# Performance work log

Hardware: AMD Instinct MI355X
Metric: run time of the kernel (lower is better)

Reference implementation:

```python
import jax, jax.numpy as jnp
import numpy as np

B, N, M, D = 256, 256, 256, 1024
BIG = 1e30  # stands in for +inf; far larger than any reachable DTW cost (<= 2*N)


def setup_inputs() -> dict:
    key = jax.random.key(0)
    k1, k2 = jax.random.split(key)
    seq1 = jax.random.normal(k1, (B, N, D), dtype=jnp.float32)
    seq2 = jax.random.normal(k2, (B, M, D), dtype=jnp.float32)
    return {"seq1": seq1, "seq2": seq2}


def _cosine_distance(x, y):
    # F.normalize(p=2, dim=2) with eps=1e-12, then 1 - clamp(x_n @ y_n^T, -1, 1)
    xn = x / jnp.maximum(jnp.linalg.norm(x, axis=2, keepdims=True), 1e-12)
    yn = y / jnp.maximum(jnp.linalg.norm(y, axis=2, keepdims=True), 1e-12)
    sim = jnp.einsum('bnd,bmd->bnm', xn, yn)
    return 1.0 - jnp.clip(sim, -1.0, 1.0)


def _dtw(dist, band_radius):
    # Banded (Sakoe-Chiba) DTW DP: acc[i,j] = d[i,j] + min(acc[i-1,j], acc[i,j-1], acc[i-1,j-1])
    # Row-wise lax.scan; within-row recurrence a[j] = min(b[j], a[j-1] + s[j]) is a
    # min-plus linear recurrence, solved in parallel with lax.associative_scan.
    b, n, m = dist.shape
    jdx = jnp.arange(m)
    # row 0: cumulative sum inside band (j <= r), BIG outside
    row0 = jnp.where(jdx[None, :] <= band_radius, jnp.cumsum(dist[:, 0, :], axis=1), BIG)

    def step(prev, xs):
        i, di = xs  # di: [b, m] = dist[:, i, :]
        in_band = (jdx >= 1) & (jdx >= i - band_radius) & (jdx <= i + band_radius)
        # column 0 only initialized while i <= band_radius (matches torch loop)
        a0 = jnp.where(i <= band_radius, prev[:, 0] + di[:, 0], BIG)
        prev_shift = jnp.concatenate([jnp.full((b, 1), BIG, dist.dtype), prev[:, :-1]], axis=1)
        c = jnp.minimum(prev, prev_shift)  # min(acc[i-1,j], acc[i-1,j-1])
        bt = jnp.where(in_band[None, :], c + di, BIG)
        st = jnp.where(in_band[None, :], di, BIG)

        def comb(l, r):
            sl, tl = l
            sr, tr = r
            return (sl + sr, jnp.minimum(tr, tl + sr))

        ss, tt = jax.lax.associative_scan(comb, (st[:, 1:], bt[:, 1:]), axis=1)
        row = jnp.concatenate([a0[:, None], jnp.minimum(tt, a0[:, None] + ss)], axis=1)
        return row, None

    xs = (jnp.arange(1, n), jnp.swapaxes(dist[:, 1:, :], 0, 1))  # ([n-1], [n-1,b,m])
    last_row, _ = jax.lax.scan(step, row0, xs)
    return last_row[:, m - 1]


def reference(seq1, seq2):
    dist = _cosine_distance(seq1, seq2)
    band_radius = min(N, M) // 2  # default: half of shorter sequence
    return _dtw(dist, band_radius)
```

## Files before the change

### kernel.cpp

```cpp
#include <hip/hip_runtime.h>
#include <hip/hip_bf16.h>

#define B_ 256
#define N_ 256
#define M_ 256
#define D_ 1024
#define RAD 128
#define BIGF 1e30f

typedef short bf16x8 __attribute__((ext_vector_type(8)));
typedef float f32x4 __attribute__((ext_vector_type(4)));

__device__ __forceinline__ short f2bf(float f) {
    __hip_bfloat16 h = __float2bfloat16(f);
    return __builtin_bit_cast(short, h);
}

__device__ __forceinline__ void cvt4(const float4 v, short* s, float& n) {
    n += v.x * v.x + v.y * v.y + v.z * v.z + v.w * v.w;
    s[0] = f2bf(v.x); s[1] = f2bf(v.y); s[2] = f2bf(v.z); s[3] = f2bf(v.w);
}

__global__ __launch_bounds__(256) void gemm_dist_kernel(
        const float* __restrict__ X, const float* __restrict__ Y,
        float* __restrict__ dist) {
    const int bid = blockIdx.x;
    const int b  = bid >> 2;
    const int ti = (bid >> 1) & 1;
    const int tj = bid & 1;

    __shared__ short As[128][32];
    __shared__ short Bs[128][32];
    __shared__ float redA[256];
    __shared__ float redB[256];
    __shared__ float rnx[128];
    __shared__ float rny[128];

    const int t    = threadIdx.x;
    const int row  = t >> 1;
    const int kh   = (t & 1) << 4;
    const int wave = t >> 6;
    const int lane = t & 63;
    const int wi   = (wave >> 1) << 6;
    const int wj   = (wave & 1) << 6;
    const int fq   = lane >> 4;
    const int fr   = lane & 15;

    const float* ax = X + (((size_t)b * N_ + ti * 128 + row) * D_) + kh;
    const float* by = Y + (((size_t)b * M_ + tj * 128 + row) * D_) + kh;

    f32x4 acc[4][4];
    const f32x4 zero = {0.f, 0.f, 0.f, 0.f};
#pragma unroll
    for (int r = 0; r < 4; ++r)
#pragma unroll
        for (int c = 0; c < 4; ++c) acc[r][c] = zero;

    float nA = 0.f, nB = 0.f;

    for (int kt = 0; kt < D_ / 32; ++kt) {
        const float4 va0 = *(const float4*)(ax + 0);
        const float4 va1 = *(const float4*)(ax + 4);
        const float4 va2 = *(const float4*)(ax + 8);
        const float4 va3 = *(const float4*)(ax + 12);
        const float4 vb0 = *(const float4*)(by + 0);
        const float4 vb1 = *(const float4*)(by + 4);
        const float4 vb2 = *(const float4*)(by + 8);
        const float4 vb3 = *(const float4*)(by + 12);
        ax += 32; by += 32;

        short sa[16], sb[16];
        cvt4(va0, sa + 0,  nA); cvt4(va1, sa + 4,  nA);
        cvt4(va2, sa + 8,  nA); cvt4(va3, sa + 12, nA);
        cvt4(vb0, sb + 0,  nB); cvt4(vb1, sb + 4,  nB);
        cvt4(vb2, sb + 8,  nB); cvt4(vb3, sb + 12, nB);

        __syncthreads();
        *(bf16x8*)&As[row][kh]     = *(bf16x8*)&sa[0];
        *(bf16x8*)&As[row][kh + 8] = *(bf16x8*)&sa[8];
        *(bf16x8*)&Bs[row][kh]     = *(bf16x8*)&sb[0];
        *(bf16x8*)&Bs[row][kh + 8] = *(bf16x8*)&sb[8];
        __syncthreads();

        bf16x8 af[4], bf[4];
#pragma unroll
        for (int r = 0; r < 4; ++r)
            af[r] = *(const bf16x8*)&As[wi + r * 16 + fr][fq * 8];
#pragma unroll
        for (int c = 0; c < 4; ++c)
            bf[c] = *(const bf16x8*)&Bs[wj + c * 16 + fr][fq * 8];
#pragma unroll
        for (int r = 0; r < 4; ++r)
#pragma unroll
            for (int c = 0; c < 4; ++c)
                acc[r][c] = __builtin_amdgcn_mfma_f32_16x16x32_bf16(
                    af[r], bf[c], acc[r][c], 0, 0, 0);
    }

    redA[t] = nA;
    redB[t] = nB;
    __syncthreads();
    if (t < 128) {
        float sA = redA[2 * t] + redA[2 * t + 1];
        float sB = redB[2 * t] + redB[2 * t + 1];
        rnx[t] = 1.0f / fmaxf(sqrtf(sA), 1e-12f);
        rny[t] = 1.0f / fmaxf(sqrtf(sB), 1e-12f);
    }
    __syncthreads();

    float* Dp = dist + (((size_t)b * N_ + ti * 128) * M_) + tj * 128;
#pragma unroll
    for (int r = 0; r < 4; ++r) {
#pragma unroll
        for (int c = 0; c < 4; ++c) {
            const int col = wj + c * 16 + fr;
            const float rc = rny[col];
#pragma unroll
            for (int g = 0; g < 4; ++g) {
                const int rw = wi + r * 16 + fq * 4 + g;
                float v = acc[r][c][g] * rnx[rw] * rc;
                v = fminf(1.0f, fmaxf(-1.0f, v));
                Dp[(size_t)rw * M_ + col] = 1.0f - v;
            }
        }
    }
}

__global__ __launch_bounds__(64) void dtw_kernel(
        const float* __restrict__ dist, float* __restrict__ out) {
    const int b = blockIdx.x;
    const int lane = threadIdx.x;
    const float* Db = dist + (size_t)b * N_ * M_;
    const int j0 = lane << 2;

    float4 d = *(const float4*)(Db + j0);
    float s0 = d.x, s1 = s0 + d.y, s2 = s1 + d.z, s3 = s2 + d.w;
    float tot = s3;
#pragma unroll
    for (int off = 1; off < 64; off <<= 1) {
        float o = __shfl_up(tot, off);
        if (lane >= off) tot += o;
    }
    float excl = __shfl_up(tot, 1);
    if (lane == 0) excl = 0.f;
    float prev[4];
    prev[0] = (j0 + 0 <= RAD) ? excl + s0 : BIGF;
    prev[1] = (j0 + 1 <= RAD) ? excl + s1 : BIGF;
    prev[2] = (j0 + 2 <= RAD) ? excl + s2 : BIGF;
    prev[3] = (j0 + 3 <= RAD) ? excl + s3 : BIGF;

    float4 dn = *(const float4*)(Db + M_ + j0);

    for (int i = 1; i < N_; ++i) {
        d = dn;
        if (i + 1 < N_) dn = *(const float4*)(Db + (size_t)(i + 1) * M_ + j0);

        const float pm1 = __shfl_up(prev[3], 1);
        const float p00 = __shfl(prev[0], 0);
        const float d00 = __shfl(d.x, 0);
        const float a0 = (i <= RAD) ? p00 + d00 : BIGF;

        const float de[4] = {d.x, d.y, d.z, d.w};
        const float ps[4] = {pm1, prev[0], prev[1], prev[2]};

        float S = 0.f, T = BIGF;
        float Se[4], Te[4];
#pragma unroll
        for (int e = 0; e < 4; ++e) {
            const int j = j0 + e;
            float st, bt;
            if (j == 0) {
                st = 0.f; bt = BIGF;
            } else {
                const bool in = (j >= i - RAD) && (j <= i + RAD);
                const float c = fminf(prev[e], ps[e]);
                bt = in ? c + de[e] : BIGF;
                st = in ? de[e] : BIGF;
            }
            T = fminf(bt, T + st);
            S = S + st;
            Se[e] = S; Te[e] = T;
        }

        float iS = S, iT = T;
#pragma unroll
        for (int off = 1; off < 64; off <<= 1) {
            float oS = __shfl_up(iS, off);
            float oT = __shfl_up(iT, off);
            if (lane >= off) {
                iT = fminf(iT, oT + iS);
                iS = oS + iS;
            }
        }
        float eS = __shfl_up(iS, 1);
        float eT = __shfl_up(iT, 1);
        if (lane == 0) { eS = 0.f; eT = BIGF; }

#pragma unroll
        for (int e = 0; e < 4; ++e) {
            const float fS = eS + Se[e];
            const float fT = fminf(Te[e], eT + Se[e]);
            prev[e] = fminf(fT, a0 + fS);
        }
        if (lane == 0) prev[0] = a0;
    }

    if (lane == 63) out[b] = prev[3];
}

extern "C" void kernel_launch(void* const* d_in, const int* in_sizes, int n_in,
                              void* d_out, int out_size, void* d_ws, size_t ws_size,
                              hipStream_t stream) {
    const float* seq1 = (const float*)d_in[0];
    const float* seq2 = (const float*)d_in[1];
    float* out = (float*)d_out;
    float* dist = (float*)d_ws;

    hipLaunchKernelGGL(gemm_dist_kernel, dim3(B_ * 4), dim3(256), 0, stream,
                       seq1, seq2, dist);
    hipLaunchKernelGGL(dtw_kernel, dim3(B_), dim3(64), 0, stream, dist, out);
}
```

Baseline: 682.4 us.

## Double-buffer padded LDS tiles and prefetch global loads in distance GEMM

The GEMM main loop now keeps two LDS buffers, unrolled two k-tiles per iteration, and needs only one barrier per tile instead of two. It also loads the next tile's global data into registers before staging the current one, so memory latency overlaps the MFMA work. LDS rows are padded from 32 to 40 shorts to cut bank conflicts on fragment reads. The norm-reduction scratch now reuses the A tile buffer to offset the larger LDS footprint. The cost is more registers held by the prefetched tiles, which may reduce occupancy.

```diff
diff --git a/kernel.cpp b/kernel.cpp
--- a/kernel.cpp
+++ b/kernel.cpp
@@ -7,6 +7,7 @@
 #define D_ 1024
 #define RAD 128
 #define BIGF 1e30f
+#define LDK 40
 
 typedef short bf16x8 __attribute__((ext_vector_type(8)));
 typedef float f32x4 __attribute__((ext_vector_type(4)));
@@ -19,6 +20,21 @@
 __device__ __forceinline__ void cvt4(const float4 v, short* s, float& n) {
     n += v.x * v.x + v.y * v.y + v.z * v.z + v.w * v.w;
     s[0] = f2bf(v.x); s[1] = f2bf(v.y); s[2] = f2bf(v.z); s[3] = f2bf(v.w);
+}
+
+struct Pk { float4 a0, a1, a2, a3, b0, b1, b2, b3; };
+
+__device__ __forceinline__ Pk loadpk(const float* ax, const float* by) {
+    Pk p;
+    p.a0 = *(const float4*)(ax + 0);
+    p.a1 = *(const float4*)(ax + 4);
+    p.a2 = *(const float4*)(ax + 8);
+    p.a3 = *(const float4*)(ax + 12);
+    p.b0 = *(const float4*)(by + 0);
+    p.b1 = *(const float4*)(by + 4);
+    p.b2 = *(const float4*)(by + 8);
+    p.b3 = *(const float4*)(by + 12);
+    return p;
 }
 
 __global__ __launch_bounds__(256) void gemm_dist_kernel(
@@ -29,12 +45,8 @@
     const int ti = (bid >> 1) & 1;
     const int tj = bid & 1;
 
-    __shared__ short As[128][32];
-    __shared__ short Bs[128][32];
-    __shared__ float redA[256];
-    __shared__ float redB[256];
-    __shared__ float rnx[128];
-    __shared__ float rny[128];
+    __shared__ alignas(16) short As[2][128][LDK];
+    __shared__ alignas(16) short Bs[2][128][LDK];
 
     const int t    = threadIdx.x;
     const int row  = t >> 1;
@@ -58,55 +70,58 @@
 
     float nA = 0.f, nB = 0.f;
 
-    for (int kt = 0; kt < D_ / 32; ++kt) {
-        const float4 va0 = *(const float4*)(ax + 0);
-        const float4 va1 = *(const float4*)(ax + 4);
-        const float4 va2 = *(const float4*)(ax + 8);
-        const float4 va3 = *(const float4*)(ax + 12);
-        const float4 vb0 = *(const float4*)(by + 0);
-        const float4 vb1 = *(const float4*)(by + 4);
-        const float4 vb2 = *(const float4*)(by + 8);
-        const float4 vb3 = *(const float4*)(by + 12);
-        ax += 32; by += 32;
-
+    auto stage = [&](const Pk& p, int buf) {
         short sa[16], sb[16];
-        cvt4(va0, sa + 0,  nA); cvt4(va1, sa + 4,  nA);
-        cvt4(va2, sa + 8,  nA); cvt4(va3, sa + 12, nA);
-        cvt4(vb0, sb + 0,  nB); cvt4(vb1, sb + 4,  nB);
-        cvt4(vb2, sb + 8,  nB); cvt4(vb3, sb + 12, nB);
-
+        cvt4(p.a0, sa + 0,  nA); cvt4(p.a1, sa + 4,  nA);
+        cvt4(p.a2, sa + 8,  nA); cvt4(p.a3, sa + 12, nA);
+        cvt4(p.b0, sb + 0,  nB); cvt4(p.b1, sb + 4,  nB);
+        cvt4(p.b2, sb + 8,  nB); cvt4(p.b3, sb + 12, nB);
+
+        *(bf16x8*)&As[buf][row][kh]     = *(bf16x8*)&sa[0];
+        *(bf16x8*)&As[buf][row][kh + 8] = *(bf16x8*)&sa[8];
+        *(bf16x8*)&Bs[buf][row][kh]     = *(bf16x8*)&sb[0];
+        *(bf16x8*)&Bs[buf][row][kh + 8] = *(bf16x8*)&sb[8];
         __syncthreads();
-        *(bf16x8*)&As[row][kh]     = *(bf16x8*)&sa[0];
-        *(bf16x8*)&As[row][kh + 8] = *(bf16x8*)&sa[8];
-        *(bf16x8*)&Bs[row][kh]     = *(bf16x8*)&sb[0];
-        *(bf16x8*)&Bs[row][kh + 8] = *(bf16x8*)&sb[8];
-        __syncthreads();
-
-        bf16x8 af[4], bf[4];
+
+        bf16x8 af[4], bfr[4];
 #pragma unroll
         for (int r = 0; r < 4; ++r)
-            af[r] = *(const bf16x8*)&As[wi + r * 16 + fr][fq * 8];
+            af[r] = *(const bf16x8*)&As[buf][wi + r * 16 + fr][fq * 8];
 #pragma unroll
         for (int c = 0; c < 4; ++c)
-            bf[c] = *(const bf16x8*)&Bs[wj + c * 16 + fr][fq * 8];
+            bfr[c] = *(const bf16x8*)&Bs[buf][wj + c * 16 + fr][fq * 8];
 #pragma unroll
         for (int r = 0; r < 4; ++r)
 #pragma unroll
             for (int c = 0; c < 4; ++c)
                 acc[r][c] = __builtin_amdgcn_mfma_f32_16x16x32_bf16(
-                    af[r], bf[c], acc[r][c], 0, 0, 0);
-    }
-
-    redA[t] = nA;
-    redB[t] = nB;
+                    af[r], bfr[c], acc[r][c], 0, 0, 0);
+    };
+
+    Pk cur = loadpk(ax, by); ax += 32; by += 32;
+    for (int kt = 0; kt < D_ / 32; kt += 2) {
+        Pk nxt = loadpk(ax, by); ax += 32; by += 32;
+        stage(cur, 0);
+        if (kt + 2 < D_ / 32) {
+            cur = loadpk(ax, by); ax += 32; by += 32;
+        }
+        stage(nxt, 1);
+    }
+
+    __syncthreads();
+    float* scratch = (float*)&As[0][0][0];
+    scratch[t]       = nA;
+    scratch[256 + t] = nB;
     __syncthreads();
     if (t < 128) {
-        float sA = redA[2 * t] + redA[2 * t + 1];
-        float sB = redB[2 * t] + redB[2 * t + 1];
-        rnx[t] = 1.0f / fmaxf(sqrtf(sA), 1e-12f);
-        rny[t] = 1.0f / fmaxf(sqrtf(sB), 1e-12f);
+        float sA = scratch[2 * t] + scratch[2 * t + 1];
+        float sB = scratch[256 + 2 * t] + scratch[256 + 2 * t + 1];
+        scratch[512 + t] = 1.0f / fmaxf(sqrtf(sA), 1e-12f);
+        scratch[640 + t] = 1.0f / fmaxf(sqrtf(sB), 1e-12f);
     }
     __syncthreads();
+    const float* rnx = scratch + 512;
+    const float* rny = scratch + 640;
 
     float* Dp = dist + (((size_t)b * N_ + ti * 128) * M_) + tj * 128;
 #pragma unroll
```

Measured after the change: 663.8 us. 1.03x faster.

## Double-buffer GEMM tiles with direct global-to-LDS loads and swizzled layout

Applied to the files above, without the earlier changes.

The distance GEMM now stages fp32 tiles straight into double-buffered shared memory with global_load_lds, prefetching the next K-slice while computing the current one. Conversion to bf16 and the row-norm accumulation move to after the LDS read, and an XOR swizzle is meant to avoid bank conflicts. Block indices are remapped across XCDs and launch bounds request two blocks per CU. The cost is fp32 LDS tiles, which doubles shared-memory use and LDS read traffic, plus redundant bf16 conversions per wave.

```diff
diff --git a/kernel.cpp b/kernel.cpp
--- a/kernel.cpp
+++ b/kernel.cpp
@@ -16,38 +16,44 @@
     return __builtin_bit_cast(short, h);
 }
 
-__device__ __forceinline__ void cvt4(const float4 v, short* s, float& n) {
-    n += v.x * v.x + v.y * v.y + v.z * v.z + v.w * v.w;
-    s[0] = f2bf(v.x); s[1] = f2bf(v.y); s[2] = f2bf(v.z); s[3] = f2bf(v.w);
-}
-
-__global__ __launch_bounds__(256) void gemm_dist_kernel(
+#define GLL16(g, l)                                                        \
+    __builtin_amdgcn_global_load_lds(                                      \
+        (const __attribute__((address_space(1))) void*)(g),                \
+        (__attribute__((address_space(3))) void*)(l), 16, 0, 0)
+
+__global__ __launch_bounds__(256, 2) void gemm_dist_kernel(
         const float* __restrict__ X, const float* __restrict__ Y,
         float* __restrict__ dist) {
-    const int bid = blockIdx.x;
+    const int obid = blockIdx.x;
+    const int bid  = (obid & 7) * (B_ * 4 / 8) + (obid >> 3);
     const int b  = bid >> 2;
     const int ti = (bid >> 1) & 1;
     const int tj = bid & 1;
 
-    __shared__ short As[128][32];
-    __shared__ short Bs[128][32];
-    __shared__ float redA[256];
-    __shared__ float redB[256];
-    __shared__ float rnx[128];
-    __shared__ float rny[128];
+    __shared__ float Asf[2][128][32];
+    __shared__ float Bsf[2][128][32];
 
     const int t    = threadIdx.x;
-    const int row  = t >> 1;
-    const int kh   = (t & 1) << 4;
     const int wave = t >> 6;
     const int lane = t & 63;
     const int wi   = (wave >> 1) << 6;
     const int wj   = (wave & 1) << 6;
     const int fq   = lane >> 4;
     const int fr   = lane & 15;
-
-    const float* ax = X + (((size_t)b * N_ + ti * 128 + row) * D_) + kh;
-    const float* by = Y + (((size_t)b * M_ + tj * 128 + row) * D_) + kh;
+    const int sA   = fr & 7;
+
+    const int lr  = lane >> 3;
+    const int lg  = lane & 7;
+    const int gsw = (lg ^ lr) << 2;
+
+    const float* gA[4];
+    const float* gB[4];
+#pragma unroll
+    for (int i = 0; i < 4; ++i) {
+        const int c = wave * 4 + i;
+        gA[i] = X + ((size_t)(b * N_ + ti * 128 + c * 8 + lr)) * D_ + gsw;
+        gB[i] = Y + ((size_t)(b * M_ + tj * 128 + c * 8 + lr)) * D_ + gsw;
+    }
 
     f32x4 acc[4][4];
     const f32x4 zero = {0.f, 0.f, 0.f, 0.f};
@@ -56,55 +62,97 @@
 #pragma unroll
         for (int c = 0; c < 4; ++c) acc[r][c] = zero;
 
-    float nA = 0.f, nB = 0.f;
-
+    float nAr[4] = {0.f, 0.f, 0.f, 0.f};
+    float nBr[4] = {0.f, 0.f, 0.f, 0.f};
+
+    const int g0f = (((fq << 1) | 0) ^ sA) << 2;
+    const int g1f = (((fq << 1) | 1) ^ sA) << 2;
+
+    auto stage = [&](int buf, int kt) {
+#pragma unroll
+        for (int i = 0; i < 4; ++i) {
+            const int c = wave * 4 + i;
+            GLL16(gA[i] + kt * 32, &Asf[buf][c * 8][0]);
+            GLL16(gB[i] + kt * 32, &Bsf[buf][c * 8][0]);
+        }
+    };
+
+    stage(0, 0);
     for (int kt = 0; kt < D_ / 32; ++kt) {
-        const float4 va0 = *(const float4*)(ax + 0);
-        const float4 va1 = *(const float4*)(ax + 4);
-        const float4 va2 = *(const float4*)(ax + 8);
-        const float4 va3 = *(const float4*)(ax + 12);
-        const float4 vb0 = *(const float4*)(by + 0);
-        const float4 vb1 = *(const float4*)(by + 4);
-        const float4 vb2 = *(const float4*)(by + 8);
-        const float4 vb3 = *(const float4*)(by + 12);
-        ax += 32; by += 32;
-
-        short sa[16], sb[16];
-        cvt4(va0, sa + 0,  nA); cvt4(va1, sa + 4,  nA);
-        cvt4(va2, sa + 8,  nA); cvt4(va3, sa + 12, nA);
-        cvt4(vb0, sb + 0,  nB); cvt4(vb1, sb + 4,  nB);
-        cvt4(vb2, sb + 8,  nB); cvt4(vb3, sb + 12, nB);
-
-        __syncthreads();
-        *(bf16x8*)&As[row][kh]     = *(bf16x8*)&sa[0];
-        *(bf16x8*)&As[row][kh + 8] = *(bf16x8*)&sa[8];
-        *(bf16x8*)&Bs[row][kh]     = *(bf16x8*)&sb[0];
-        *(bf16x8*)&Bs[row][kh + 8] = *(bf16x8*)&sb[8];
-        __syncthreads();
-
-        bf16x8 af[4], bf[4];
-#pragma unroll
-        for (int r = 0; r < 4; ++r)
-            af[r] = *(const bf16x8*)&As[wi + r * 16 + fr][fq * 8];
-#pragma unroll
-        for (int c = 0; c < 4; ++c)
-            bf[c] = *(const bf16x8*)&Bs[wj + c * 16 + fr][fq * 8];
+        const int buf = kt & 1;
+        if (kt + 1 < D_ / 32) {
+            stage(buf ^ 1, kt + 1);
+            asm volatile("s_waitcnt vmcnt(8)" ::: "memory");
+        } else {
+            asm volatile("s_waitcnt vmcnt(0)" ::: "memory");
+        }
+        __builtin_amdgcn_s_barrier();
+        asm volatile("" ::: "memory");
+
+        const float (*Ab)[32] = Asf[buf];
+        const float (*Bb)[32] = Bsf[buf];
+
+        bf16x8 af[4], bfv[4];
+#pragma unroll
+        for (int r = 0; r < 4; ++r) {
+            const float* rp = &Ab[wi + r * 16 + fr][0];
+            const f32x4 lo = *(const f32x4*)(rp + g0f);
+            const f32x4 hi = *(const f32x4*)(rp + g1f);
+            if (wj == 0) {
+                nAr[r] += lo[0]*lo[0] + lo[1]*lo[1] + lo[2]*lo[2] + lo[3]*lo[3]
+                        + hi[0]*hi[0] + hi[1]*hi[1] + hi[2]*hi[2] + hi[3]*hi[3];
+            }
+            bf16x8 v;
+            v[0]=f2bf(lo[0]); v[1]=f2bf(lo[1]); v[2]=f2bf(lo[2]); v[3]=f2bf(lo[3]);
+            v[4]=f2bf(hi[0]); v[5]=f2bf(hi[1]); v[6]=f2bf(hi[2]); v[7]=f2bf(hi[3]);
+            af[r] = v;
+        }
+#pragma unroll
+        for (int c = 0; c < 4; ++c) {
+            const float* rp = &Bb[wj + c * 16 + fr][0];
+            const f32x4 lo = *(const f32x4*)(rp + g0f);
+            const f32x4 hi = *(const f32x4*)(rp + g1f);
+            if (wi == 0) {
+                nBr[c] += lo[0]*lo[0] + lo[1]*lo[1] + lo[2]*lo[2] + lo[3]*lo[3]
+                        + hi[0]*hi[0] + hi[1]*hi[1] + hi[2]*hi[2] + hi[3]*hi[3];
+            }
+            bf16x8 v;
+            v[0]=f2bf(lo[0]); v[1]=f2bf(lo[1]); v[2]=f2bf(lo[2]); v[3]=f2bf(lo[3]);
+            v[4]=f2bf(hi[0]); v[5]=f2bf(hi[1]); v[6]=f2bf(hi[2]); v[7]=f2bf(hi[3]);
+            bfv[c] = v;
+        }
+
 #pragma unroll
         for (int r = 0; r < 4; ++r)
 #pragma unroll
             for (int c = 0; c < 4; ++c)
                 acc[r][c] = __builtin_amdgcn_mfma_f32_16x16x32_bf16(
-                    af[r], bf[c], acc[r][c], 0, 0, 0);
-    }
-
-    redA[t] = nA;
-    redB[t] = nB;
+                    af[r], bfv[c], acc[r][c], 0, 0, 0);
+
+        asm volatile("" ::: "memory");
+        __builtin_amdgcn_s_barrier();
+    }
+
     __syncthreads();
-    if (t < 128) {
-        float sA = redA[2 * t] + redA[2 * t + 1];
-        float sB = redB[2 * t] + redB[2 * t + 1];
-        rnx[t] = 1.0f / fmaxf(sqrtf(sA), 1e-12f);
-        rny[t] = 1.0f / fmaxf(sqrtf(sB), 1e-12f);
+    float* rnx = (float*)&Asf[0][0][0];
+    float* rny = rnx + 128;
+    if (wj == 0) {
+#pragma unroll
+        for (int r = 0; r < 4; ++r) {
+            float s = nAr[r];
+            s += __shfl_xor(s, 16);
+            s += __shfl_xor(s, 32);
+            if (fq == 0) rnx[wi + r * 16 + fr] = 1.0f / fmaxf(sqrtf(s), 1e-12f);
+        }
+    }
+    if (wi == 0) {
+#pragma unroll
+        for (int c = 0; c < 4; ++c) {
+            float s = nBr[c];
+            s += __shfl_xor(s, 16);
+            s += __shfl_xor(s, 32);
+            if (fq == 0) rny[wj + c * 16 + fr] = 1.0f / fmaxf(sqrtf(s), 1e-12f);
+        }
     }
     __syncthreads();
 
```

Measured after the change: 641.0 us. 1.06x faster.
